# Kernel tuning notes

Hardware: AMD Instinct MI355X
Metric: run time of the kernel (lower is better)

Reference implementation:

```python
import jax, jax.numpy as jnp
import numpy as np

N_NODES = 100000
D = 128
N_EDGES = 800000


def setup_inputs() -> dict:
    key = jax.random.key(0)
    k_feat, k_src, k_dst, k_ws, k_wn = jax.random.split(key, 5)
    scale = 1.0 / np.sqrt(D)
    return {
        "features": jax.random.normal(k_feat, (N_NODES, D), jnp.float32),
        "src": jax.random.randint(k_src, (N_EDGES,), 0, N_NODES, jnp.int32),
        "dst": jax.random.randint(k_dst, (N_EDGES,), 0, N_NODES, jnp.int32),
        "gamma": jnp.ones((D,), jnp.float32),
        "beta": jnp.zeros((D,), jnp.float32),
        "W_self": jax.random.normal(k_ws, (D, D), jnp.float32) * scale,
        "W_neigh": jax.random.normal(k_wn, (D, D), jnp.float32) * scale,
        "b": jnp.zeros((D,), jnp.float32),
    }


def reference(features, src, dst, gamma, beta, W_self, W_neigh, b):
    n = features.shape[0]
    eps = 1e-5
    # BatchNorm1d (training mode: batch stats over the node dim, biased var)
    mean = jnp.mean(features, axis=0)
    var = jnp.mean(jnp.square(features - mean), axis=0)
    h = (features - mean) * jax.lax.rsqrt(var + eps) * gamma + beta  # [N, D]

    # SAGEConv 'mean': gather source feats along edges, mean-reduce per dst node
    msg = h[src]  # [E, D] irregular gather
    agg = jax.ops.segment_sum(msg, dst, num_segments=n)  # [N, D]
    deg = jax.ops.segment_sum(jnp.ones(src.shape, h.dtype), dst, num_segments=n)
    h_neigh = agg / jnp.maximum(deg, 1.0)[:, None]  # zero-degree nodes stay 0

    conv = h @ W_self + h_neigh @ W_neigh + b  # fc_self + fc_neigh + bias
    out = conv + h  # skip connection
    return jax.nn.gelu(out, approximate=False)
```

## Files before the change

### kernel.cpp

```cpp
#include <hip/hip_runtime.h>

#define DD 128
#define NPB_LOG 8
#define NPB 256
#define EPB 2048

typedef __attribute__((ext_vector_type(8))) short short8;
typedef __attribute__((ext_vector_type(4))) float f32x4;
typedef __attribute__((ext_vector_type(2))) float f32x2;

__device__ inline unsigned short f2bf(float f) {
    unsigned u = __float_as_uint(f);
    unsigned r = u + 0x7fffu + ((u >> 16) & 1u);
    return (unsigned short)(r >> 16);
}
__device__ inline float bf2f(unsigned short s) {
    return __uint_as_float(((unsigned)s) << 16);
}

__global__ __launch_bounds__(256) void phase1_k(
    const float4* __restrict__ x, float* __restrict__ stats16, int n,
    const int* __restrict__ dst, int nE, int NCHUNK, int NBUCK,
    const float* __restrict__ Wself, const float* __restrict__ Wneigh,
    unsigned short* __restrict__ Bpre, int* __restrict__ cm) {
    int b = blockIdx.x, tid = threadIdx.x;
    __shared__ float ls[8][256];
    if (b < 16) {
        int q = b * 256 + tid;
        int l = q & 63;
        int kb = ((q >> 9) << 5) + ((l >> 4) << 3);
        int nn = (((q >> 6) & 7) << 4) + (l & 15);
        bool self = (kb < 128);
        const float* Wp = self ? (Wself + (size_t)kb * 128 + nn)
                               : (Wneigh + (size_t)(kb - 128) * 128 + nn);
        unsigned tmp[4];
#pragma unroll
        for (int j = 0; j < 4; ++j) {
            float v0 = Wp[(2 * j) * 128];
            float v1 = Wp[(2 * j + 1) * 128];
            if (self) {
                if (kb + 2 * j == nn) v0 += 1.0f;
                if (kb + 2 * j + 1 == nn) v1 += 1.0f;
            }
            tmp[j] = (unsigned)f2bf(v0) | ((unsigned)f2bf(v1) << 16);
        }
        uint4 w; w.x = tmp[0]; w.y = tmp[1]; w.z = tmp[2]; w.w = tmp[3];
        *(uint4*)(Bpre + (size_t)q * 8) = w;
    } else if (b < 16 + 1024) {
        int bb = b - 16;
        int c4 = tid & 31, sub = tid >> 5;
        float sx = 0.f, sy = 0.f, sz = 0.f, sw = 0.f;
        float qx = 0.f, qy = 0.f, qz = 0.f, qw = 0.f;
        for (int r = bb * 8 + sub; r < n; r += 1024 * 8) {
            float4 v = x[(size_t)r * 32 + c4];
            sx += v.x; sy += v.y; sz += v.z; sw += v.w;
            qx += v.x * v.x; qy += v.y * v.y; qz += v.z * v.z; qw += v.w * v.w;
        }
        ls[sub][c4 * 4 + 0] = sx; ls[sub][c4 * 4 + 1] = sy;
        ls[sub][c4 * 4 + 2] = sz; ls[sub][c4 * 4 + 3] = sw;
        ls[sub][128 + c4 * 4 + 0] = qx; ls[sub][128 + c4 * 4 + 1] = qy;
        ls[sub][128 + c4 * 4 + 2] = qz; ls[sub][128 + c4 * 4 + 3] = qw;
        __syncthreads();
        float t = 0.f;
#pragma unroll
        for (int k = 0; k < 8; ++k) t += ls[k][tid];
        atomicAdd(&stats16[(bb & 15) * 256 + tid], t);
    } else {
        int chunk = b - 1040;
        int* cnt = (int*)ls;
        for (int i = tid; i < NBUCK; i += 256) cnt[i] = 0;
        __syncthreads();
        int e0 = chunk * EPB;
#pragma unroll
        for (int j = 0; j < 8; ++j) {
            int e = e0 + j * 256 + tid;
            if (e < nE) atomicAdd(&cnt[dst[e] >> NPB_LOG], 1);
        }
        __syncthreads();
        for (int bk = tid; bk < NBUCK; bk += 256)
            cm[(size_t)bk * NCHUNK + chunk] = cnt[bk];
    }
}

__global__ __launch_bounds__(256) void scanA_k(
    const int* __restrict__ v_in, int* __restrict__ bsum, int n) {
    int b = blockIdx.x, t = threadIdx.x;
    int i0 = b * 1024 + t * 4;
    int4 v = {0, 0, 0, 0};
    if (i0 + 3 < n) v = *(const int4*)(v_in + i0);
    else {
        if (i0 < n) v.x = v_in[i0];
        if (i0 + 1 < n) v.y = v_in[i0 + 1];
        if (i0 + 2 < n) v.z = v_in[i0 + 2];
    }
    __shared__ int ls[256];
    ls[t] = v.x + v.y + v.z + v.w;
    __syncthreads();
#pragma unroll
    for (int off = 128; off > 0; off >>= 1) {
        if (t < off) ls[t] += ls[t + off];
        __syncthreads();
    }
    if (t == 0) bsum[b] = ls[0];
}

__global__ __launch_bounds__(256) void scanB_k(
    const int* __restrict__ bsum, int* __restrict__ bpref,
    int* __restrict__ total_out, int nb, int n) {
    __shared__ int ls[256];
    int t = threadIdx.x;
    ls[t] = (t < nb) ? bsum[t] : 0;
    __syncthreads();
#pragma unroll
    for (int off = 1; off < 256; off <<= 1) {
        int x = (t >= off) ? ls[t - off] : 0;
        __syncthreads();
        ls[t] += x;
        __syncthreads();
    }
    if (t < nb) bpref[t] = (t == 0) ? 0 : ls[t - 1];
    if (t == nb - 1) total_out[n] = ls[t];
}

__global__ __launch_bounds__(256) void scanC_k(
    const int* __restrict__ v_in, const int* __restrict__ bpref,
    int* __restrict__ o1, int* __restrict__ o2, int n) {
    int b = blockIdx.x, t = threadIdx.x;
    int i0 = b * 1024 + t * 4;
    int4 v = {0, 0, 0, 0};
    if (i0 + 3 < n) v = *(const int4*)(v_in + i0);
    else {
        if (i0 < n) v.x = v_in[i0];
        if (i0 + 1 < n) v.y = v_in[i0 + 1];
        if (i0 + 2 < n) v.z = v_in[i0 + 2];
    }
    int s = v.x + v.y + v.z + v.w;
    __shared__ int ls[256];
    ls[t] = s;
    __syncthreads();
#pragma unroll
    for (int off = 1; off < 256; off <<= 1) {
        int x = (t >= off) ? ls[t - off] : 0;
        __syncthreads();
        ls[t] += x;
        __syncthreads();
    }
    int run = bpref[b] + ((t == 0) ? 0 : ls[t - 1]);
    int4 o;
    o.x = run; o.y = run + v.x; o.z = o.y + v.y; o.w = o.z + v.z;
    if (i0 + 3 < n) {
        *(int4*)(o1 + i0) = o;
        *(int4*)(o2 + i0) = o;
    } else {
        if (i0 < n) { o1[i0] = o.x; o2[i0] = o.x; }
        if (i0 + 1 < n) { o1[i0 + 1] = o.y; o2[i0 + 1] = o.y; }
        if (i0 + 2 < n) { o1[i0 + 2] = o.z; o2[i0 + 2] = o.z; }
    }
}

__global__ __launch_bounds__(256) void phase2_k(
    const float4* __restrict__ x, const float* __restrict__ stats16,
    const float4* __restrict__ gamma, const float4* __restrict__ beta,
    uint2* __restrict__ hbuf, unsigned* __restrict__ h8, int n, float inv_n,
    int nbNorm, const int* __restrict__ src, const int* __restrict__ dst,
    const int* __restrict__ cmscan, unsigned* __restrict__ pairs,
    int nE, int NCHUNK, int NBUCK) {
    int b = blockIdx.x, tid = threadIdx.x;
    __shared__ int shr[512];
    if (b < nbNorm) {
        float* fs = (float*)shr;
        float a = 0.f;
#pragma unroll
        for (int sh = 0; sh < 16; ++sh) a += stats16[sh * 256 + tid];
        fs[tid] = a;
        __syncthreads();
        int c4 = tid & 31, sub = tid >> 5;
        int row = b * 8 + sub;
        float4 sm = ((const float4*)fs)[c4], sq = ((const float4*)fs)[32 + c4];
        float4 g = gamma[c4], bt = beta[c4];
        float mx = sm.x * inv_n, my = sm.y * inv_n, mz = sm.z * inv_n, mw = sm.w * inv_n;
        float vx = sq.x * inv_n - mx * mx, vy = sq.y * inv_n - my * my;
        float vz = sq.z * inv_n - mz * mz, vw = sq.w * inv_n - mw * mw;
        float scx = rsqrtf(vx + 1e-5f) * g.x, scy = rsqrtf(vy + 1e-5f) * g.y;
        float scz = rsqrtf(vz + 1e-5f) * g.z, scw = rsqrtf(vw + 1e-5f) * g.w;
        float shx = bt.x - mx * scx, shy = bt.y - my * scy;
        float shz = bt.z - mz * scz, shw = bt.w - mw * scw;
        if (row < n) {
            float4 v = x[(size_t)row * 32 + c4];
            float hx = v.x * scx + shx, hy = v.y * scy + shy;
            float hz = v.z * scz + shz, hw = v.w * scw + shw;
            uint2 o;
            o.x = (unsigned)f2bf(hx) | ((unsigned)f2bf(hy) << 16);
            o.y = (unsigned)f2bf(hz) | ((unsigned)f2bf(hw) << 16);
            hbuf[(size_t)row * 32 + c4] = o;
            int p8 = __builtin_amdgcn_cvt_pk_fp8_f32(hx, hy, 0, false);
            p8 = __builtin_amdgcn_cvt_pk_fp8_f32(hz, hw, p8, true);
            h8[(size_t)row * 32 + c4] = (unsigned)p8;
        }
    } else {
        int chunk = b - nbNorm;
        for (int i = tid; i < NBUCK; i += 256)
            shr[i] = cmscan[(size_t)i * NCHUNK + chunk];
        __syncthreads();
        int e0 = chunk * EPB;
#pragma unroll
        for (int j = 0; j < 8; ++j) {
            int e = e0 + j * 256 + tid;
            if (e < nE) {
                int d = dst[e];
                int p = atomicAdd(&shr[d >> NPB_LOG], 1);
                pairs[p] = ((unsigned)src[e] << NPB_LOG) | (unsigned)(d & (NPB - 1));
            }
        }
    }
}

__global__ __launch_bounds__(256) void sortC_k(
    const unsigned* __restrict__ pairs, const int* __restrict__ cmscan,
    int* __restrict__ offsets, int* __restrict__ csr,
    int n, int nE, int NCHUNK, int NBUCK) {
    int b = blockIdx.x, tid = threadIdx.x;
    int base0 = cmscan[(size_t)b * NCHUNK];
    int end = (b + 1 < NBUCK) ? cmscan[(size_t)(b + 1) * NCHUNK] : nE;
    __shared__ int cnt[NPB];
    __shared__ int cur[NPB];
    cnt[tid] = 0;
    __syncthreads();
    for (int e = base0 + tid; e < end; e += 256)
        atomicAdd(&cnt[pairs[e] & (NPB - 1)], 1);
    __syncthreads();
    int c0 = cnt[tid];
    __shared__ int ps[256];
    ps[tid] = c0;
    __syncthreads();
#pragma unroll
    for (int off = 1; off < 256; off <<= 1) {
        int v = (tid >= off) ? ps[tid - off] : 0;
        __syncthreads();
        ps[tid] += v;
        __syncthreads();
    }
    int ex = base0 + ps[tid] - c0;
    cur[tid] = ex;
    int node = b * NPB + tid;
    if (node < n) offsets[node] = ex;
    if (b == NBUCK - 1 && tid == 0) offsets[n] = nE;
    __syncthreads();
    for (int e = base0 + tid; e < end; e += 256) {
        unsigned u = pairs[e];
        int p = atomicAdd(&cur[u & (NPB - 1)], 1);
        csr[p] = (int)(u >> NPB_LOG);
    }
}

#define ACC8(v)                                                       \
    do {                                                              \
        acc[0] += __builtin_amdgcn_cvt_pk_f32_fp8((v).x, false);      \
        acc[1] += __builtin_amdgcn_cvt_pk_f32_fp8((v).x, true);       \
        acc[2] += __builtin_amdgcn_cvt_pk_f32_fp8((v).y, false);      \
        acc[3] += __builtin_amdgcn_cvt_pk_f32_fp8((v).y, true);       \
        acc[4] += __builtin_amdgcn_cvt_pk_f32_fp8((v).z, false);      \
        acc[5] += __builtin_amdgcn_cvt_pk_f32_fp8((v).z, true);       \
        acc[6] += __builtin_amdgcn_cvt_pk_f32_fp8((v).w, false);      \
        acc[7] += __builtin_amdgcn_cvt_pk_f32_fp8((v).w, true);       \
    } while (0)

__global__ __launch_bounds__(256) void pull_k(
    const int* __restrict__ offsets, const int* __restrict__ csr,
    const uint4* __restrict__ h8q, uint4* __restrict__ hnw, int n) {
    int wv = (blockIdx.x * 256 + threadIdx.x) >> 6;
    int lane = threadIdx.x & 63;
    int g = lane >> 3, sl = lane & 7;
    int node = wv * 8 + g;
    bool valid = node < n;
    int nc = valid ? node : (n - 1);
    int b0 = offsets[nc], b1 = offsets[nc + 1];
    f32x2 acc[8];
#pragma unroll
    for (int k = 0; k < 8; ++k) acc[k] = f32x2{0.f, 0.f};
    int j = b0;
    for (; j + 4 <= b1; j += 4) {
        int i0 = csr[j], i1 = csr[j + 1], i2 = csr[j + 2], i3 = csr[j + 3];
        uint4 v0 = h8q[(size_t)i0 * 8 + sl];
        uint4 v1 = h8q[(size_t)i1 * 8 + sl];
        uint4 v2 = h8q[(size_t)i2 * 8 + sl];
        uint4 v3 = h8q[(size_t)i3 * 8 + sl];
        ACC8(v0); ACC8(v1); ACC8(v2); ACC8(v3);
    }
    if (j + 2 <= b1) {
        int i0 = csr[j], i1 = csr[j + 1];
        uint4 v0 = h8q[(size_t)i0 * 8 + sl];
        uint4 v1 = h8q[(size_t)i1 * 8 + sl];
        ACC8(v0); ACC8(v1);
        j += 2;
    }
    if (j < b1) {
        int i0 = csr[j];
        uint4 v0 = h8q[(size_t)i0 * 8 + sl];
        ACC8(v0);
    }
    if (valid) {
        float rd = (b1 > b0) ? 1.0f / (float)(b1 - b0) : 0.0f;
        unsigned ow[8];
#pragma unroll
        for (int k = 0; k < 8; ++k)
            ow[k] = (unsigned)f2bf(acc[k].x * rd) |
                    ((unsigned)f2bf(acc[k].y * rd) << 16);
        uint4 o1; o1.x = ow[0]; o1.y = ow[1]; o1.z = ow[2]; o1.w = ow[3];
        uint4 o2; o2.x = ow[4]; o2.y = ow[5]; o2.z = ow[6]; o2.w = ow[7];
        hnw[(size_t)node * 16 + sl * 2] = o1;
        hnw[(size_t)node * 16 + sl * 2 + 1] = o2;
    }
}

__global__ __launch_bounds__(256, 4) void gemm_k(
    const unsigned short* __restrict__ h, const unsigned short* __restrict__ hn,
    const unsigned short* __restrict__ Bpre, const float* __restrict__ bias,
    float* __restrict__ out, int n) {
    __shared__ unsigned short Bsw[16384];
    int tid = threadIdx.x, wave = tid >> 6, lane = tid & 63;
    int H = blockIdx.x & 1, rb = blockIdx.x >> 1;
#pragma unroll
    for (int i = 0; i < 8; ++i) {
        int g = wave * 8 + i;
        int s = g >> 2, tt = g & 3;
        __builtin_amdgcn_global_load_lds(
            (const __attribute__((address_space(1))) void*)(
                Bpre + ((size_t)((s * 8 + H * 4 + tt) * 64) + lane) * 8),
            (__attribute__((address_space(3))) void*)(Bsw + (size_t)g * 512),
            16, 0, 0);
    }
    __syncthreads();

    int quad = lane >> 4, mrow = lane & 15;
    int r0 = rb * 128 + wave * 32;
    int rA0 = min(r0 + mrow, n - 1);
    int rA1 = min(r0 + 16 + mrow, n - 1);

    f32x4 zero = {0.0f, 0.0f, 0.0f, 0.0f};
    f32x4 acc[2][4];
#pragma unroll
    for (int m = 0; m < 2; ++m)
#pragma unroll
        for (int t = 0; t < 4; ++t) acc[m][t] = zero;

#pragma unroll
    for (int s = 0; s < 8; ++s) {
        int kb = s * 32 + quad * 8;
        short8 a0, a1;
        if (s < 4) {
            a0 = *(const short8*)(h + (size_t)rA0 * 128 + kb);
            a1 = *(const short8*)(h + (size_t)rA1 * 128 + kb);
        } else {
            int kk = kb - 128;
            a0 = *(const short8*)(hn + (size_t)rA0 * 128 + kk);
            a1 = *(const short8*)(hn + (size_t)rA1 * 128 + kk);
        }
#pragma unroll
        for (int tt = 0; tt < 4; ++tt) {
            short8 b = *(const short8*)(Bsw + ((size_t)(s * 4 + tt) * 64 + lane) * 8);
            acc[0][tt] = __builtin_amdgcn_mfma_f32_16x16x32_bf16(a0, b, acc[0][tt], 0, 0, 0);
            acc[1][tt] = __builtin_amdgcn_mfma_f32_16x16x32_bf16(a1, b, acc[1][tt], 0, 0, 0);
        }
    }

    float bi[4];
#pragma unroll
    for (int t = 0; t < 4; ++t) bi[t] = bias[H * 64 + t * 16 + mrow];
#pragma unroll
    for (int m = 0; m < 2; ++m) {
#pragma unroll
        for (int i = 0; i < 4; ++i) {
            int row = r0 + m * 16 + quad * 4 + i;
            if (row < n) {
#pragma unroll
                for (int t = 0; t < 4; ++t) {
                    int col = H * 64 + t * 16 + mrow;
                    float xv = acc[m][t][i] + bi[t];
                    float x2 = xv * xv;
                    float u = 0.7978845608f * xv * (1.0f + 0.044715f * x2);
                    float e = __expf(2.0f * u);
                    float th = 1.0f - 2.0f * __builtin_amdgcn_rcpf(e + 1.0f);
                    out[(size_t)row * 128 + col] = 0.5f * xv * (1.0f + th);
                }
            }
        }
    }
}

extern "C" void kernel_launch(void* const* d_in, const int* in_sizes, int n_in,
                              void* d_out, int out_size, void* d_ws, size_t ws_size,
                              hipStream_t stream) {
    const float* features = (const float*)d_in[0];
    const int* src = (const int*)d_in[1];
    const int* dst = (const int*)d_in[2];
    const float* gamma = (const float*)d_in[3];
    const float* beta = (const float*)d_in[4];
    const float* Wself = (const float*)d_in[5];
    const float* Wneigh = (const float*)d_in[6];
    const float* bias = (const float*)d_in[7];
    int n = in_sizes[0] / DD;
    int nE = in_sizes[1];
    int NCHUNK = (nE + EPB - 1) / EPB;
    int NBUCK = (n + NPB - 1) / NPB;
    int CM = NBUCK * NCHUNK;
    int tilesCM = (CM + 1023) / 1024;
    int nbNorm = (n + 7) / 8;

    auto align1k = [](size_t x) { return (x + 1023) & ~(size_t)1023; };
    char* ws = (char*)d_ws;
    size_t off = 0;
    float* stats16 = (float*)(ws + off);       off += 16384;
    int* cm       = (int*)(ws + off);          off += align1k((size_t)(CM + 1) * 4);
    int* cmscan   = (int*)(ws + off);          off += align1k((size_t)CM * 4);
    int* offsets  = (int*)(ws + off);          off += align1k((size_t)(n + 1) * 4);
    int* csr      = (int*)(ws + off);          off += align1k((size_t)nE * 4);
    unsigned* pairs = (unsigned*)(ws + off);   off += align1k((size_t)nE * 4);
    int* bsum     = (int*)(ws + off);          off += 1024;
    int* bpref    = (int*)(ws + off);          off += 1024;
    unsigned short* Bpre = (unsigned short*)(ws + off); off += 65536;
    unsigned short* hbuf = (unsigned short*)(ws + off); off += (size_t)n * 256;
    unsigned short* hnbuf = (unsigned short*)(ws + off); off += (size_t)n * 256;
    unsigned* h8 = (unsigned*)(ws + off);      off += (size_t)n * 128;

    hipMemsetAsync(stats16, 0, 16384, stream);

    phase1_k<<<16 + 1024 + NCHUNK, 256, 0, stream>>>(
        (const float4*)features, stats16, n, dst, nE, NCHUNK, NBUCK,
        Wself, Wneigh, Bpre, cm);
    scanA_k<<<tilesCM, 256, 0, stream>>>(cm, bsum, CM);
    scanB_k<<<1, 256, 0, stream>>>(bsum, bpref, cm, tilesCM, CM);
    scanC_k<<<tilesCM, 256, 0, stream>>>(cm, bpref, cmscan, cmscan, CM);
    phase2_k<<<nbNorm + NCHUNK, 256, 0, stream>>>(
        (const float4*)features, stats16, (const float4*)gamma,
        (const float4*)beta, (uint2*)hbuf, h8, n, 1.0f / (float)n, nbNorm,
        src, dst, cmscan, pairs, nE, NCHUNK, NBUCK);
    sortC_k<<<NBUCK, 256, 0, stream>>>(pairs, cmscan, offsets, csr, n, nE,
                                       NCHUNK, NBUCK);
    {
        int waves = (n + 7) / 8;
        int blocks = (waves * 64 + 255) / 256;
        pull_k<<<blocks, 256, 0, stream>>>(
            offsets, csr, (const uint4*)h8, (uint4*)hnbuf, n);
    }
    gemm_k<<<((n + 127) / 128) * 2, 256, 0, stream>>>(
        hbuf, hnbuf, Bpre, bias, (float*)d_out, n);
}
```

Before: 207.8 us.

## Precompute BatchNorm scale/shift once and widen GEMM tiles to full output width

BatchNorm mean/variance reduction and scale/shift computation move into the single-block scanB kernel, writing a 256-float scale/shift table. The normalize blocks in phase2 then read that table instead of each re-reducing the 16 partial stat slices and recomputing rsqrt. The GEMM kernel now computes all 128 output columns per block instead of splitting into two column halves, so the A operands (h and h_neigh) are loaded once rather than twice. The cost is twice the LDS for the weights and twice the accumulator registers, with launch bounds lowered from 4 to 2 blocks per CU.

```diff
diff --git a/kernel.cpp b/kernel.cpp
--- a/kernel.cpp
+++ b/kernel.cpp
@@ -106,9 +106,24 @@
 
 __global__ __launch_bounds__(256) void scanB_k(
     const int* __restrict__ bsum, int* __restrict__ bpref,
-    int* __restrict__ total_out, int nb, int n) {
+    int* __restrict__ total_out, int nb, int n,
+    const float* __restrict__ stats16, const float* __restrict__ gamma,
+    const float* __restrict__ beta, float* __restrict__ scsh, float inv_n) {
+    int t = threadIdx.x;
+    if (t < 128) {
+        float s = 0.f, q = 0.f;
+#pragma unroll
+        for (int sh = 0; sh < 16; ++sh) {
+            s += stats16[sh * 256 + t];
+            q += stats16[sh * 256 + 128 + t];
+        }
+        float mean = s * inv_n;
+        float var = q * inv_n - mean * mean;
+        float sc = rsqrtf(var + 1e-5f) * gamma[t];
+        scsh[t] = sc;
+        scsh[128 + t] = beta[t] - mean * sc;
+    }
     __shared__ int ls[256];
-    int t = threadIdx.x;
     ls[t] = (t < nb) ? bsum[t] : 0;
     __syncthreads();
 #pragma unroll
@@ -159,36 +174,22 @@
 }
 
 __global__ __launch_bounds__(256) void phase2_k(
-    const float4* __restrict__ x, const float* __restrict__ stats16,
-    const float4* __restrict__ gamma, const float4* __restrict__ beta,
-    uint2* __restrict__ hbuf, unsigned* __restrict__ h8, int n, float inv_n,
+    const float4* __restrict__ x, const float* __restrict__ scsh,
+    uint2* __restrict__ hbuf, unsigned* __restrict__ h8, int n,
     int nbNorm, const int* __restrict__ src, const int* __restrict__ dst,
     const int* __restrict__ cmscan, unsigned* __restrict__ pairs,
     int nE, int NCHUNK, int NBUCK) {
     int b = blockIdx.x, tid = threadIdx.x;
     __shared__ int shr[512];
     if (b < nbNorm) {
-        float* fs = (float*)shr;
-        float a = 0.f;
-#pragma unroll
-        for (int sh = 0; sh < 16; ++sh) a += stats16[sh * 256 + tid];
-        fs[tid] = a;
-        __syncthreads();
         int c4 = tid & 31, sub = tid >> 5;
         int row = b * 8 + sub;
-        float4 sm = ((const float4*)fs)[c4], sq = ((const float4*)fs)[32 + c4];
-        float4 g = gamma[c4], bt = beta[c4];
-        float mx = sm.x * inv_n, my = sm.y * inv_n, mz = sm.z * inv_n, mw = sm.w * inv_n;
-        float vx = sq.x * inv_n - mx * mx, vy = sq.y * inv_n - my * my;
-        float vz = sq.z * inv_n - mz * mz, vw = sq.w * inv_n - mw * mw;
-        float scx = rsqrtf(vx + 1e-5f) * g.x, scy = rsqrtf(vy + 1e-5f) * g.y;
-        float scz = rsqrtf(vz + 1e-5f) * g.z, scw = rsqrtf(vw + 1e-5f) * g.w;
-        float shx = bt.x - mx * scx, shy = bt.y - my * scy;
-        float shz = bt.z - mz * scz, shw = bt.w - mw * scw;
+        float4 sc = ((const float4*)scsh)[c4];
+        float4 sh = ((const float4*)(scsh + 128))[c4];
         if (row < n) {
             float4 v = x[(size_t)row * 32 + c4];
-            float hx = v.x * scx + shx, hy = v.y * scy + shy;
-            float hz = v.z * scz + shz, hw = v.w * scw + shw;
+            float hx = v.x * sc.x + sh.x, hy = v.y * sc.y + sh.y;
+            float hz = v.z * sc.z + sh.z, hw = v.w * sc.w + sh.w;
             uint2 o;
             o.x = (unsigned)f2bf(hx) | ((unsigned)f2bf(hy) << 16);
             o.y = (unsigned)f2bf(hz) | ((unsigned)f2bf(hw) << 16);
@@ -313,20 +314,19 @@
     }
 }
 
-__global__ __launch_bounds__(256, 4) void gemm_k(
+__global__ __launch_bounds__(256, 2) void gemm_k(
     const unsigned short* __restrict__ h, const unsigned short* __restrict__ hn,
     const unsigned short* __restrict__ Bpre, const float* __restrict__ bias,
     float* __restrict__ out, int n) {
-    __shared__ unsigned short Bsw[16384];
+    __shared__ unsigned short Bsw[32768];
     int tid = threadIdx.x, wave = tid >> 6, lane = tid & 63;
-    int H = blockIdx.x & 1, rb = blockIdx.x >> 1;
-#pragma unroll
-    for (int i = 0; i < 8; ++i) {
-        int g = wave * 8 + i;
-        int s = g >> 2, tt = g & 3;
+    int rb = blockIdx.x;
+#pragma unroll
+    for (int i = 0; i < 16; ++i) {
+        int g = wave * 16 + i;
         __builtin_amdgcn_global_load_lds(
             (const __attribute__((address_space(1))) void*)(
-                Bpre + ((size_t)((s * 8 + H * 4 + tt) * 64) + lane) * 8),
+                Bpre + ((size_t)g * 64 + lane) * 8),
             (__attribute__((address_space(3))) void*)(Bsw + (size_t)g * 512),
             16, 0, 0);
     }
@@ -338,11 +338,11 @@
     int rA1 = min(r0 + 16 + mrow, n - 1);
 
     f32x4 zero = {0.0f, 0.0f, 0.0f, 0.0f};
-    f32x4 acc[2][4];
+    f32x4 acc[2][8];
 #pragma unroll
     for (int m = 0; m < 2; ++m)
 #pragma unroll
-        for (int t = 0; t < 4; ++t) acc[m][t] = zero;
+        for (int t = 0; t < 8; ++t) acc[m][t] = zero;
 
 #pragma unroll
     for (int s = 0; s < 8; ++s) {
@@ -357,16 +357,16 @@
             a1 = *(const short8*)(hn + (size_t)rA1 * 128 + kk);
         }
 #pragma unroll
-        for (int tt = 0; tt < 4; ++tt) {
-            short8 b = *(const short8*)(Bsw + ((size_t)(s * 4 + tt) * 64 + lane) * 8);
+        for (int tt = 0; tt < 8; ++tt) {
+            short8 b = *(const short8*)(Bsw + ((size_t)(s * 8 + tt) * 64 + lane) * 8);
             acc[0][tt] = __builtin_amdgcn_mfma_f32_16x16x32_bf16(a0, b, acc[0][tt], 0, 0, 0);
             acc[1][tt] = __builtin_amdgcn_mfma_f32_16x16x32_bf16(a1, b, acc[1][tt], 0, 0, 0);
         }
     }
 
-    float bi[4];
-#pragma unroll
-    for (int t = 0; t < 4; ++t) bi[t] = bias[H * 64 + t * 16 + mrow];
+    float bi[8];
+#pragma unroll
+    for (int t = 0; t < 8; ++t) bi[t] = bias[t * 16 + mrow];
 #pragma unroll
     for (int m = 0; m < 2; ++m) {
 #pragma unroll
@@ -374,8 +374,8 @@
             int row = r0 + m * 16 + quad * 4 + i;
             if (row < n) {
 #pragma unroll
-                for (int t = 0; t < 4; ++t) {
-                    int col = H * 64 + t * 16 + mrow;
+                for (int t = 0; t < 8; ++t) {
+                    int col = t * 16 + mrow;
                     float xv = acc[m][t][i] + bi[t];
                     float x2 = xv * xv;
                     float u = 0.7978845608f * xv * (1.0f + 0.044715f * x2);
@@ -411,6 +411,7 @@
     char* ws = (char*)d_ws;
     size_t off = 0;
     float* stats16 = (float*)(ws + off);       off += 16384;
+    float* scsh   = (float*)(ws + off);        off += 2048;
     int* cm       = (int*)(ws + off);          off += align1k((size_t)(CM + 1) * 4);
     int* cmscan   = (int*)(ws + off);          off += align1k((size_t)CM * 4);
     int* offsets  = (int*)(ws + off);          off += align1k((size_t)(n + 1) * 4);
@@ -429,11 +430,11 @@
         (const float4*)features, stats16, n, dst, nE, NCHUNK, NBUCK,
         Wself, Wneigh, Bpre, cm);
     scanA_k<<<tilesCM, 256, 0, stream>>>(cm, bsum, CM);
-    scanB_k<<<1, 256, 0, stream>>>(bsum, bpref, cm, tilesCM, CM);
+    scanB_k<<<1, 256, 0, stream>>>(bsum, bpref, cm, tilesCM, CM,
+                                   stats16, gamma, beta, scsh, 1.0f / (float)n);
     scanC_k<<<tilesCM, 256, 0, stream>>>(cm, bpref, cmscan, cmscan, CM);
     phase2_k<<<nbNorm + NCHUNK, 256, 0, stream>>>(
-        (const float4*)features, stats16, (const float4*)gamma,
-        (const float4*)beta, (uint2*)hbuf, h8, n, 1.0f / (float)n, nbNorm,
+        (const float4*)features, scsh, (uint2*)hbuf, h8, n, nbNorm,
         src, dst, cmscan, pairs, nE, NCHUNK, NBUCK);
     sortC_k<<<NBUCK, 256, 0, stream>>>(pairs, cmscan, offsets, csr, n, nE,
                                        NCHUNK, NBUCK);
@@ -443,6 +444,6 @@
         pull_k<<<blocks, 256, 0, stream>>>(
             offsets, csr, (const uint4*)h8, (uint4*)hnbuf, n);
     }
-    gemm_k<<<((n + 127) / 128) * 2, 256, 0, stream>>>(
+    gemm_k<<<(n + 127) / 128, 256, 0, stream>>>(
         hbuf, hnbuf, Bpre, bias, (float*)d_out, n);
 }
```

After: 195.7 us. 5.9% less time.
